# Performance work log

Hardware: AMD Instinct MI355X
Metric: run time of the kernel (lower is better)

The kernel has to match this reference:

```python
import jax, jax.numpy as jnp
import numpy as np

B, T, S = 128, 256, 64
IN, H, K, CSL, OUT = 3, 512, 10, 60, 121


def setup_inputs() -> dict:
    key = jax.random.key(0)
    ks = jax.random.split(key, 10)
    s = lambda k, shape, sc: jax.random.normal(k, shape, jnp.float32) * sc
    return {
        "x": jax.random.normal(ks[0], (B, T, IN), jnp.float32),
        "sentences": jax.random.uniform(ks[1], (B, S, CSL), dtype=jnp.float32),
        "h1_h": jnp.zeros((B, H), jnp.float32),
        "h1_c": jnp.zeros((B, H), jnp.float32),
        "h2_h": jnp.zeros((B, H), jnp.float32),
        "h2_c": jnp.zeros((B, H), jnp.float32),
        # LSTMCell params (torch gate order i,f,g,o); b = b_ih + b_hh fused
        "W_ih_cell": s(ks[2], (4 * H, IN + CSL), 0.04),
        "W_hh_cell": s(ks[3], (4 * H, H), 0.04),
        "b_cell": jnp.zeros((4 * H,), jnp.float32),
        # second-layer nn.LSTM params
        "W_ih_l": s(ks[4], (4 * H, IN + CSL + H), 0.04),
        "W_hh_l": s(ks[5], (4 * H, H), 0.04),
        "b_l": jnp.zeros((4 * H,), jnp.float32),
        # fc1 -> window params, fc2 -> output
        "W1": s(ks[6], (3 * K, H), 0.04),
        "b1": jnp.zeros((3 * K,), jnp.float32),
        "W2": s(ks[7], (OUT, H), 0.04),
        "b2": jnp.zeros((OUT,), jnp.float32),
    }


def _lstm_step(h, c, xt, W_ih, W_hh, b):
    g = xt @ W_ih.T + h @ W_hh.T + b
    i, f, gg, o = jnp.split(g, 4, axis=-1)
    c2 = jax.nn.sigmoid(f) * c + jax.nn.sigmoid(i) * jnp.tanh(gg)
    h2 = jax.nn.sigmoid(o) * jnp.tanh(c2)
    return h2, c2


def reference(x, sentences, h1_h, h1_c, h2_h, h2_c,
              W_ih_cell, W_hh_cell, b_cell,
              W_ih_l, W_hh_l, b_l, W1, b1, W2, b2):
    u = jnp.arange(1, S + 1, dtype=x.dtype)[:, None]  # [S,1] char positions

    def step1(carry, xt):
        h, c, p = carry
        ip = jnp.exp(h @ W1.T + b1)                                     # [B,3K]
        # kappa part subtracts the previous step's kappa (quirk of the source)
        p_new = jnp.concatenate([ip[:, :2 * K], ip[:, 2 * K:] - p[:, 2 * K:]], axis=-1)
        a, be, ka = jnp.split(p_new[:, None, :], 3, axis=-1)            # each [B,1,K]
        phi = (a * jnp.exp(-be * (ka - u) ** 2)).sum(-1)                # [B,S]
        win = jnp.einsum('bs,bsc->bc', phi, sentences)                  # [B,CSL]
        h2, c2 = _lstm_step(h, c, jnp.concatenate([xt, win], axis=-1),
                            W_ih_cell, W_hh_cell, b_cell)
        return (h2, c2, p_new), (h2, win)

    xs = jnp.swapaxes(x, 0, 1)                                          # [T,B,IN]
    p0 = jnp.zeros((x.shape[0], 3 * K), x.dtype)
    (h1f, c1f, _), (hx, wins) = jax.lax.scan(step1, (h1_h, h1_c, p0), xs)

    feat = jnp.concatenate([xs, wins, hx], axis=-1)                     # [T,B,IN+CSL+H]

    def step2(carry, xt):
        h, c = carry
        h2, c2 = _lstm_step(h, c, xt, W_ih_l, W_hh_l, b_l)
        return (h2, c2), h2

    (h2f, c2f), ys = jax.lax.scan(step2, (h2_h, h2_c), feat)
    y = jnp.swapaxes(ys, 0, 1).reshape(-1, H)                           # [B*T,H]
    out = y @ W2.T + b2                                                 # [B*T,OUT]
    return out, h1f, c1f, h2f, c2f
```

## Files before the change

### kernel.cpp

```cpp
#include <hip/hip_runtime.h>
#include <hip/hip_bf16.h>
#include <math.h>

typedef __attribute__((ext_vector_type(8))) short short8;
typedef __attribute__((ext_vector_type(4))) float floatx4;

#define DEVFN static __device__ __forceinline__

constexpr int B = 128, T = 256, H = 512;
constexpr int OUTW = 121;
constexpr int SLOTW = 1664;
constexpr int LOOF  = 1088;
constexpr int SLOTE = B * SLOTW;
constexpr int NSLOT = T + 2;
constexpr int NG  = 2048;
constexpr int K1  = 576,  K1C = 18;
constexpr int K2  = 1088, K2C = 34;
constexpr int KW1P = 584, KW2P = 1096;

constexpr int O_WH1 = 0;
constexpr int O_WL1 = 37376;
constexpr int O_W1S = 74752;
constexpr int O_GSM = 137152;
constexpr int O_HS  = 137152;
constexpr int O_PP  = 139264;
constexpr int O_IPL = 145472;
constexpr int O_KL  = 145592;
constexpr int O_PHL = 145632;
constexpr int O_WAC = 145888;
constexpr int O_KPR = 146848;
constexpr int O_B1S = 146888;
constexpr int O_BIA = 147008;
constexpr int O_SENT = 147136;
constexpr int O_WH2 = 0;
constexpr int O_WL2 = 70144;
constexpr int O_GS2 = 140288;
constexpr int O_BI2 = 148608;
constexpr int LDS_SZ = 162496;

DEVFN __hip_bfloat16 bhi(float v) { return __float2bfloat16(v); }
DEVFN __hip_bfloat16 blo(float v, __hip_bfloat16 h) { return __float2bfloat16(v - __bfloat162float(h)); }
DEVFN float bf2f(__hip_bfloat16 h) { return __bfloat162float(h); }
DEVFN unsigned short bbits(__hip_bfloat16 h) { union { __hip_bfloat16 h; unsigned short u; } c; c.h = h; return c.u; }
DEVFN unsigned int pack2(float a, float b) {
  return (unsigned int)bbits(bhi(a)) | ((unsigned int)bbits(bhi(b)) << 16);
}
DEVFN void ast(unsigned int* p, unsigned int v) {
  __hip_atomic_store(p, v, __ATOMIC_RELAXED, __HIP_MEMORY_SCOPE_AGENT);
}
DEVFN int ald(int* p) {
  return __hip_atomic_load(p, __ATOMIC_RELAXED, __HIP_MEMORY_SCOPE_AGENT);
}

DEVFN void waitflags(int* flags, int n, int target) {
  if ((int)threadIdx.x < n) {
    int g = 0;
    while (ald(&flags[threadIdx.x]) < target && g < (1 << 22)) { ++g; __builtin_amdgcn_s_sleep(1); }
  }
  asm volatile("" ::: "memory");
  __syncthreads();
}
DEVFN void dualwait(int* fa, int* fb, int target) {
  int tid = threadIdx.x;
  if (tid < 128) {
    int* f = (tid < 64) ? fa + tid : fb + (tid - 64);
    int g = 0;
    while (ald(f) < target && g < (1 << 22)) { ++g; __builtin_amdgcn_s_sleep(1); }
  }
  asm volatile("" ::: "memory");
  __syncthreads();
}
DEVFN void flag_store(int* flag, int val) {
  asm volatile("s_waitcnt vmcnt(0)" ::: "memory");
  __syncthreads();
  if (threadIdx.x == 0)
    __hip_atomic_store(flag, val, __ATOMIC_RELAXED, __HIP_MEMORY_SCOPE_AGENT);
}

__global__ __launch_bounds__(256) void k_pre(
    const float* __restrict__ x, const float* __restrict__ h1h, const float* __restrict__ h2h,
    const float* __restrict__ Wihc, const float* __restrict__ Whhc, const float* __restrict__ bc,
    const float* __restrict__ Wihl, const float* __restrict__ Whhl, const float* __restrict__ bl,
    const float* __restrict__ W2,
    __hip_bfloat16* __restrict__ fxHL,
    __hip_bfloat16* __restrict__ wc1, __hip_bfloat16* __restrict__ wc1l,
    __hip_bfloat16* __restrict__ wc2, __hip_bfloat16* __restrict__ wc2l,
    __hip_bfloat16* __restrict__ w2b, float* __restrict__ bi1, float* __restrict__ bi2,
    int* __restrict__ ctl)
{
  int idx = blockIdx.x * 256 + threadIdx.x;
  const int nwc1 = NG * K1, nwc2 = NG * K2, nw2b = 128 * 512, nbi = 2 * NG;
  const int nfh = B * H, nxj = T * B, nctl = 512;
  if (idx < nwc1) {
    int n = idx / K1, col = idx - n * K1;
    int src = (n & 3) * H + (n >> 2);
    float v = (col < 63) ? Wihc[src * 63 + col]
            : (col == 63 ? 0.f : Whhc[src * 512 + (col - 64)]);
    __hip_bfloat16 h = bhi(v);
    wc1[n * K1 + col] = h; wc1l[n * K1 + col] = blo(v, h);
    return;
  }
  idx -= nwc1;
  if (idx < nwc2) {
    int n = idx / K2, col = idx - n * K2;
    int src = (n & 3) * H + (n >> 2);
    float v;
    if (col < 63)       v = Wihl[src * 575 + col];
    else if (col == 63) v = 0.f;
    else if (col < 576) v = Wihl[src * 575 + (col - 1)];
    else                v = Whhl[src * 512 + (col - 576)];
    __hip_bfloat16 h = bhi(v);
    wc2[n * K2 + col] = h; wc2l[n * K2 + col] = blo(v, h);
    return;
  }
  idx -= nwc2;
  if (idx < nw2b) {
    int n = idx >> 9, col = idx & 511;
    w2b[idx] = bhi(n < OUTW ? W2[n * 512 + col] : 0.f);
    return;
  }
  idx -= nw2b;
  if (idx < nbi) {
    int n = idx & (NG - 1);
    int src = (n & 3) * H + (n >> 2);
    if (idx < NG) bi1[n] = bc[src]; else bi2[n] = bl[src];
    return;
  }
  idx -= nbi;
  if (idx < nfh) {
    int b = idx >> 9, j = idx & 511;
    float v = h1h[idx];
    __hip_bfloat16 h = bhi(v);
    fxHL[b * SLOTW + 64 + j] = h;
    fxHL[b * SLOTW + LOOF + 64 + j] = blo(v, h);
    return;
  }
  idx -= nfh;
  if (idx < nfh) {
    int b = idx >> 9, j = idx & 511;
    fxHL[(size_t)SLOTE + b * SLOTW + 576 + j] = bhi(h2h[idx]);
    return;
  }
  idx -= nfh;
  if (idx < nxj) {
    int t = idx >> 7, b = idx & 127;
    float x0 = x[(b * T + t) * 3 + 0], x1 = x[(b * T + t) * 3 + 1];
    unsigned int* ph = (unsigned int*)(fxHL + (size_t)(t + 1) * SLOTE + b * SLOTW);
    ph[0] = pack2(x0, x1);
    unsigned int* pl = (unsigned int*)(fxHL + (size_t)(t + 1) * SLOTE + b * SLOTW + LOOF);
    pl[0] = 0u;
    return;
  }
  idx -= nxj;
  if (idx < nctl) ctl[idx] = 0;
}

template <int KWP>
DEVFN void gemm3(int tid, const __hip_bfloat16* __restrict__ Aslot, int m0,
                 const __hip_bfloat16* __restrict__ Wh, const __hip_bfloat16* __restrict__ Wl,
                 int cbeg, int cend, floatx4& a0, floatx4& a1)
{
  const int lane = tid & 63, wv = tid >> 6;
  const int lm = lane & 15, lk = (lane >> 4) << 3;
  const __hip_bfloat16* Ar = Aslot + (size_t)(m0 + wv * 16 + lm) * SLOTW;
  const __hip_bfloat16* W0h = Wh + lm * KWP;
  const __hip_bfloat16* W1h = Wh + (16 + lm) * KWP;
  const __hip_bfloat16* W0l = Wl + lm * KWP;
  const __hip_bfloat16* W1l = Wl + (16 + lm) * KWP;
  #pragma unroll 4
  for (int c = cbeg; c < cend; ++c) {
    int col = c * 32 + lk;
    short8 va  = *(const short8*)(Ar + col);
    short8 ua  = *(const short8*)(Ar + LOOF + col);
    short8 vb0 = *(const short8*)(W0h + col);
    short8 vb1 = *(const short8*)(W1h + col);
    short8 ub0 = *(const short8*)(W0l + col);
    short8 ub1 = *(const short8*)(W1l + col);
    a0 = __builtin_amdgcn_mfma_f32_16x16x32_bf16(va, vb0, a0, 0, 0, 0);
    a1 = __builtin_amdgcn_mfma_f32_16x16x32_bf16(va, vb1, a1, 0, 0, 0);
    a0 = __builtin_amdgcn_mfma_f32_16x16x32_bf16(va, ub0, a0, 0, 0, 0);
    a1 = __builtin_amdgcn_mfma_f32_16x16x32_bf16(va, ub1, a1, 0, 0, 0);
    a0 = __builtin_amdgcn_mfma_f32_16x16x32_bf16(ua, vb0, a0, 0, 0, 0);
    a1 = __builtin_amdgcn_mfma_f32_16x16x32_bf16(ua, vb1, a1, 0, 0, 0);
  }
}

DEVFN void store_gsm(int tid, float* Gsm, floatx4 a0, floatx4 a1) {
  const int lane = tid & 63, wv = tid >> 6;
  const int lm = lane & 15, rr = (lane >> 4) << 2;
  #pragma unroll
  for (int r = 0; r < 4; ++r) {
    Gsm[lm * 65 + wv * 16 + rr + r]        = a0[r];
    Gsm[(16 + lm) * 65 + wv * 16 + rr + r] = a1[r];
  }
}

__global__ __launch_bounds__(256, 1) void k_persist(
    __hip_bfloat16* __restrict__ fxHL,
    const __hip_bfloat16* __restrict__ wc1, const __hip_bfloat16* __restrict__ wc1l,
    const __hip_bfloat16* __restrict__ wc2, const __hip_bfloat16* __restrict__ wc2l,
    const float* __restrict__ bi1, const float* __restrict__ bi2,
    const float* __restrict__ c1init, const float* __restrict__ c2init,
    const float* __restrict__ xin, const float* __restrict__ sent,
    const float* __restrict__ W1, const float* __restrict__ b1,
    int* __restrict__ ctl,
    float* __restrict__ h1f, float* __restrict__ c1f,
    float* __restrict__ h2f, float* __restrict__ c2f)
{
  extern __shared__ char sm[];
  const int gid = blockIdx.x, tid = threadIdx.x;
  const int lane = tid & 63, wv = tid >> 6;
  const int lm = lane & 15, lk = (lane >> 4) << 3;

  if (gid < 128) {
    const int nt1 = gid >> 1, mh = gid & 1;
    const int n0 = nt1 * 32, m0 = mh * 64;
    const int brow = mh * 64 + nt1;
    int* wf = ctl + mh * 64;
    int* hf = ctl + 128 + mh * 64;
    __hip_bfloat16* smWh = (__hip_bfloat16*)(sm + O_WH1);
    __hip_bfloat16* smWl = (__hip_bfloat16*)(sm + O_WL1);
    float* smW1 = (float*)(sm + O_W1S);
    float* Gsm  = (float*)(sm + O_GSM);
    float* hs   = (float*)(sm + O_HS);
    float* winv = (float*)(sm + O_HS);
    float* pp   = (float*)(sm + O_PP);
    float* ipl  = (float*)(sm + O_IPL);
    float* kl   = (float*)(sm + O_KL);
    float* phl  = (float*)(sm + O_PHL);
    float* wac  = (float*)(sm + O_WAC);
    float* kpr  = (float*)(sm + O_KPR);
    float* b1s  = (float*)(sm + O_B1S);
    float* bia  = (float*)(sm + O_BIA);
    float* ssent = (float*)(sm + O_SENT);

    for (int i = tid; i < 32 * 72; i += 256) {
      int r = i / 72, c8 = (i - r * 72) * 8;
      *(short8*)(smWh + r * KW1P + c8) = *(const short8*)(wc1  + (size_t)(n0 + r) * K1 + c8);
      *(short8*)(smWl + r * KW1P + c8) = *(const short8*)(wc1l + (size_t)(n0 + r) * K1 + c8);
    }
    for (int i = tid; i < 30 * 512; i += 256) {
      int j = i >> 9, c = i & 511;
      smW1[j * 520 + (c >> 6) * 65 + (c & 63)] = W1[i];
    }
    for (int i = tid; i < 64 * 60; i += 256)
      ssent[i] = sent[(size_t)brow * 64 * 60 + i];
    if (tid < 30) b1s[tid] = b1[tid];
    if (tid < 10) kpr[tid] = 0.f;
    if (tid < 32) bia[tid] = bi1[n0 + tid];
    __syncthreads();

    float creg[2];
    {
      int ml = tid >> 2, ppi = tid & 3;
      creg[0] = c1init[(m0 + ml) * H + nt1 * 8 + 2 * ppi + 0];
      creg[1] = c1init[(m0 + ml) * H + nt1 * 8 + 2 * ppi + 1];
    }

    const __hip_bfloat16* W0h = smWh + lm * KW1P;
    const __hip_bfloat16* W1h = smWh + (16 + lm) * KW1P;
    const __hip_bfloat16* W0l = smWl + lm * KW1P;
    const __hip_bfloat16* W1l = smWl + (16 + lm) * KW1P;

    for (int t = 0; t < T; ++t) {
      __hip_bfloat16* S1 = fxHL + (size_t)(t + 1) * SLOTE;
      __hip_bfloat16* S0 = fxHL + (size_t)t * SLOTE;

      waitflags(hf, 64, t);

      const __hip_bfloat16* wrow = S0 + (size_t)brow * SLOTW;
      __hip_bfloat16 a0h = wrow[64 + tid];
      __hip_bfloat16 a0l = wrow[LOOF + 64 + tid];
      __hip_bfloat16 a1h = wrow[64 + 256 + tid];
      __hip_bfloat16 a1l = wrow[LOOF + 64 + 256 + tid];
      float x2v = xin[(brow * T + t) * 3 + 2];
      const __hip_bfloat16* Ar = S0 + (size_t)(m0 + wv * 16 + lm) * SLOTW;
      short8 pva[16], pua[16];
      #pragma unroll
      for (int c = 0; c < 16; ++c) {
        pva[c] = *(const short8*)(Ar + (c + 2) * 32 + lk);
        pua[c] = *(const short8*)(Ar + LOOF + (c + 2) * 32 + lk);
      }
      hs[(tid >> 6) * 66 + (tid & 63)] = bf2f(a0h) + bf2f(a0l);
      hs[((tid + 256) >> 6) * 66 + (tid & 63)] = bf2f(a1h) + bf2f(a1l);
      __syncthreads();

      if (tid < 240) {
        int j = tid >> 3, p = tid & 7;
        const float* wp = smW1 + j * 520 + p * 65;
        const float* hv = hs + p * 66;
        float s = 0.f;
        #pragma unroll 8
        for (int k = 0; k < 64; ++k) s += hv[k] * wp[k];
        pp[tid] = s;
      }
      __syncthreads();
      if (tid < 30) {
        float s = b1s[tid];
        #pragma unroll
        for (int p = 0; p < 8; ++p) s += pp[tid * 8 + p];
        ipl[tid] = expf(s);
      }
      __syncthreads();
      if (tid < 10) {
        float kap = ipl[20 + tid] - kpr[tid];
        kpr[tid] = kap; kl[tid] = kap;
      }
      __syncthreads();
      if (tid < 64) {
        float u = (float)(tid + 1);
        float acc = 0.f;
        #pragma unroll
        for (int k = 0; k < 10; ++k) {
          float d = kl[k] - u;
          acc += ipl[k] * expf(-ipl[10 + k] * d * d);
        }
        phl[tid] = acc;
      }
      __syncthreads();
      if (tid < 240) {
        int c = tid >> 2, p = tid & 3;
        float acc = 0.f;
        #pragma unroll
        for (int s0 = 0; s0 < 16; ++s0)
          acc += phl[p * 16 + s0] * ssent[(p * 16 + s0) * 60 + c];
        wac[tid] = acc;
      }
      __syncthreads();
      if (tid < 60)
        winv[tid] = wac[tid * 4] + wac[tid * 4 + 1] + wac[tid * 4 + 2] + wac[tid * 4 + 3];
      __syncthreads();
      if (tid < 31) {
        int d = 1 + tid;
        int c0 = 2 * d, c1 = 2 * d + 1;
        float v0 = (c0 == 2) ? x2v : winv[c0 - 3];
        float v1 = (c1 == 63) ? 0.f : winv[c1 - 3];
        __hip_bfloat16 h0 = bhi(v0), h1v = bhi(v1);
        unsigned int* prow = (unsigned int*)(S1 + (size_t)brow * SLOTW);
        ast(prow + d, (unsigned int)bbits(h0) | ((unsigned int)bbits(h1v) << 16));
        ast(prow + (LOOF >> 1) + d,
            (unsigned int)bbits(blo(v0, h0)) | ((unsigned int)bbits(blo(v1, h1v)) << 16));
      }
      flag_store(wf + nt1, t + 1);

      floatx4 a0 = {0.f, 0.f, 0.f, 0.f}, a1 = a0;
      #pragma unroll
      for (int c = 0; c < 16; ++c) {
        int col = (c + 2) * 32 + lk;
        short8 vb0 = *(const short8*)(W0h + col);
        short8 vb1 = *(const short8*)(W1h + col);
        short8 ub0 = *(const short8*)(W0l + col);
        short8 ub1 = *(const short8*)(W1l + col);
        a0 = __builtin_amdgcn_mfma_f32_16x16x32_bf16(pva[c], vb0, a0, 0, 0, 0);
        a1 = __builtin_amdgcn_mfma_f32_16x16x32_bf16(pva[c], vb1, a1, 0, 0, 0);
        a0 = __builtin_amdgcn_mfma_f32_16x16x32_bf16(pva[c], ub0, a0, 0, 0, 0);
        a1 = __builtin_amdgcn_mfma_f32_16x16x32_bf16(pva[c], ub1, a1, 0, 0, 0);
        a0 = __builtin_amdgcn_mfma_f32_16x16x32_bf16(pua[c], vb0, a0, 0, 0, 0);
        a1 = __builtin_amdgcn_mfma_f32_16x16x32_bf16(pua[c], vb1, a1, 0, 0, 0);
      }
      waitflags(wf, 64, t + 1);
      gemm3<KW1P>(tid, S1, m0, smWh, smWl, 0, 2, a0, a1);
      store_gsm(tid, Gsm, a0, a1);
      __syncthreads();

      {
        int ml = tid >> 2, ppi = tid & 3;
        float v[2];
        #pragma unroll
        for (int j = 0; j < 2; ++j) {
          int nl = ppi * 8 + j * 4;
          float gi = Gsm[(nl + 0) * 65 + ml] + bia[nl + 0];
          float gf = Gsm[(nl + 1) * 65 + ml] + bia[nl + 1];
          float gg = Gsm[(nl + 2) * 65 + ml] + bia[nl + 2];
          float go = Gsm[(nl + 3) * 65 + ml] + bia[nl + 3];
          float ig = 1.f / (1.f + expf(-gi));
          float fg = 1.f / (1.f + expf(-gf));
          float gt = tanhf(gg);
          float og = 1.f / (1.f + expf(-go));
          float cn = fg * creg[j] + ig * gt;
          v[j] = og * tanhf(cn);
          creg[j] = cn;
        }
        __hip_bfloat16 h0 = bhi(v[0]), h1v = bhi(v[1]);
        unsigned int* prow = (unsigned int*)(S1 + (size_t)(m0 + ml) * SLOTW);
        int dw = 32 + nt1 * 4 + ppi;
        ast(prow + dw, (unsigned int)bbits(h0) | ((unsigned int)bbits(h1v) << 16));
        ast(prow + (LOOF >> 1) + dw,
            (unsigned int)bbits(blo(v[0], h0)) | ((unsigned int)bbits(blo(v[1], h1v)) << 16));
        if (t == T - 1) {
          int hg = nt1 * 8 + 2 * ppi;
          h1f[(m0 + ml) * H + hg]     = v[0];  c1f[(m0 + ml) * H + hg]     = creg[0];
          h1f[(m0 + ml) * H + hg + 1] = v[1];  c1f[(m0 + ml) * H + hg + 1] = creg[1];
        }
      }
      flag_store(hf + nt1, t + 1);
    }
  } else {
    const int g = gid - 128;
    const int nt2 = g >> 1, mh = g & 1;
    const int n0 = nt2 * 32, m0 = mh * 64;
    int* wf  = ctl + mh * 64;
    int* hf  = ctl + 128 + mh * 64;
    int* h2g = ctl + 256 + mh * 64;
    __hip_bfloat16* smWh = (__hip_bfloat16*)(sm + O_WH2);
    __hip_bfloat16* smWl = (__hip_bfloat16*)(sm + O_WL2);
    float* Gsm = (float*)(sm + O_GS2);
    float* bia = (float*)(sm + O_BI2);

    for (int i = tid; i < 32 * 136; i += 256) {
      int r = i / 136, c8 = (i - r * 136) * 8;
      *(short8*)(smWh + r * KW2P + c8) = *(const short8*)(wc2  + (size_t)(n0 + r) * K2 + c8);
      *(short8*)(smWl + r * KW2P + c8) = *(const short8*)(wc2l + (size_t)(n0 + r) * K2 + c8);
    }
    if (tid < 32) bia[tid] = bi2[n0 + tid];
    __syncthreads();

    float creg[2];
    {
      int ml = tid >> 2, ppi = tid & 3;
      creg[0] = c2init[(m0 + ml) * H + nt2 * 8 + 2 * ppi + 0];
      creg[1] = c2init[(m0 + ml) * H + nt2 * 8 + 2 * ppi + 1];
    }

    const __hip_bfloat16* W0h = smWh + lm * KW2P;
    const __hip_bfloat16* W1h = smWh + (16 + lm) * KW2P;
    const __hip_bfloat16* W0l = smWl + lm * KW2P;
    const __hip_bfloat16* W1l = smWl + (16 + lm) * KW2P;

    for (int t = 0; t < T; ++t) {
      __hip_bfloat16* S1 = fxHL + (size_t)(t + 1) * SLOTE;
      __hip_bfloat16* S2 = fxHL + (size_t)(t + 2) * SLOTE;
      const __hip_bfloat16* Ar = S1 + (size_t)(m0 + wv * 16 + lm) * SLOTW;

      waitflags(h2g, 64, t);
      short8 pv2[16];
      #pragma unroll
      for (int c = 0; c < 16; ++c)
        pv2[c] = *(const short8*)(Ar + (K1C + c) * 32 + lk);
      floatx4 a0 = {0.f, 0.f, 0.f, 0.f}, a1 = a0;
      #pragma unroll
      for (int c = 0; c < 16; ++c) {
        int col = (K1C + c) * 32 + lk;
        short8 vb0 = *(const short8*)(W0h + col);
        short8 vb1 = *(const short8*)(W1h + col);
        short8 ub0 = *(const short8*)(W0l + col);
        short8 ub1 = *(const short8*)(W1l + col);
        a0 = __builtin_amdgcn_mfma_f32_16x16x32_bf16(pv2[c], vb0, a0, 0, 0, 0);
        a1 = __builtin_amdgcn_mfma_f32_16x16x32_bf16(pv2[c], vb1, a1, 0, 0, 0);
        a0 = __builtin_amdgcn_mfma_f32_16x16x32_bf16(pv2[c], ub0, a0, 0, 0, 0);
        a1 = __builtin_amdgcn_mfma_f32_16x16x32_bf16(pv2[c], ub1, a1, 0, 0, 0);
      }
      dualwait(hf, wf, t + 1);
      short8 qv[18], qu[18];
      #pragma unroll
      for (int c = 0; c < 18; ++c) {
        qv[c] = *(const short8*)(Ar + c * 32 + lk);
        qu[c] = *(const short8*)(Ar + LOOF + c * 32 + lk);
      }
      #pragma unroll
      for (int c = 0; c < 18; ++c) {
        int col = c * 32 + lk;
        short8 vb0 = *(const short8*)(W0h + col);
        short8 vb1 = *(const short8*)(W1h + col);
        short8 ub0 = *(const short8*)(W0l + col);
        short8 ub1 = *(const short8*)(W1l + col);
        a0 = __builtin_amdgcn_mfma_f32_16x16x32_bf16(qv[c], vb0, a0, 0, 0, 0);
        a1 = __builtin_amdgcn_mfma_f32_16x16x32_bf16(qv[c], vb1, a1, 0, 0, 0);
        a0 = __builtin_amdgcn_mfma_f32_16x16x32_bf16(qv[c], ub0, a0, 0, 0, 0);
        a1 = __builtin_amdgcn_mfma_f32_16x16x32_bf16(qv[c], ub1, a1, 0, 0, 0);
        a0 = __builtin_amdgcn_mfma_f32_16x16x32_bf16(qu[c], vb0, a0, 0, 0, 0);
        a1 = __builtin_amdgcn_mfma_f32_16x16x32_bf16(qu[c], vb1, a1, 0, 0, 0);
      }
      store_gsm(tid, Gsm, a0, a1);
      __syncthreads();

      {
        int ml = tid >> 2, ppi = tid & 3;
        float v[2];
        #pragma unroll
        for (int j = 0; j < 2; ++j) {
          int nl = ppi * 8 + j * 4;
          float gi = Gsm[(nl + 0) * 65 + ml] + bia[nl + 0];
          float gf = Gsm[(nl + 1) * 65 + ml] + bia[nl + 1];
          float gg = Gsm[(nl + 2) * 65 + ml] + bia[nl + 2];
          float go = Gsm[(nl + 3) * 65 + ml] + bia[nl + 3];
          float ig = 1.f / (1.f + expf(-gi));
          float fg = 1.f / (1.f + expf(-gf));
          float gt = tanhf(gg);
          float og = 1.f / (1.f + expf(-go));
          float cn = fg * creg[j] + ig * gt;
          v[j] = og * tanhf(cn);
          creg[j] = cn;
        }
        __hip_bfloat16 h0 = bhi(v[0]), h1v = bhi(v[1]);
        unsigned int* prow = (unsigned int*)(S2 + (size_t)(m0 + ml) * SLOTW);
        int dw = 288 + nt2 * 4 + ppi;
        ast(prow + dw, (unsigned int)bbits(h0) | ((unsigned int)bbits(h1v) << 16));
        if (t == T - 1) {
          int hg = nt2 * 8 + 2 * ppi;
          h2f[(m0 + ml) * H + hg]     = v[0];  c2f[(m0 + ml) * H + hg]     = creg[0];
          h2f[(m0 + ml) * H + hg + 1] = v[1];  c2f[(m0 + ml) * H + hg + 1] = creg[1];
        }
      }
      flag_store(h2g + nt2, t + 1);
    }
  }
}

__global__ __launch_bounds__(256) void k_out(
    const __hip_bfloat16* __restrict__ fxHL, const __hip_bfloat16* __restrict__ w2b,
    const float* __restrict__ b2, float* __restrict__ dout)
{
  int bid = blockIdx.x, tid = threadIdx.x;
  int mblk = bid >> 1, nblk = bid & 1;
  int wv = tid >> 6, lane = tid & 63;
  int lm = lane & 15, lk = (lane >> 4) << 3;
  int m0 = mblk * 128 + wv * 32;
  int n0 = nblk * 64;
  int r0 = m0 + lm, r1 = m0 + 16 + lm;
  const __hip_bfloat16* a0p = fxHL + (size_t)((r0 & 255) + 2) * SLOTE + (r0 >> 8) * SLOTW + 576;
  const __hip_bfloat16* a1p = fxHL + (size_t)((r1 & 255) + 2) * SLOTE + (r1 >> 8) * SLOTW + 576;
  floatx4 zz = {0.f, 0.f, 0.f, 0.f};
  floatx4 acc[2][4];
  #pragma unroll
  for (int mt = 0; mt < 2; ++mt)
    #pragma unroll
    for (int nt = 0; nt < 4; ++nt) acc[mt][nt] = zz;
  #pragma unroll
  for (int c = 0; c < 16; ++c) {
    int col = c * 32 + lk;
    short8 va0 = *(const short8*)(a0p + col);
    short8 va1 = *(const short8*)(a1p + col);
    short8 vb[4];
    #pragma unroll
    for (int nt = 0; nt < 4; ++nt)
      vb[nt] = *(const short8*)(w2b + (size_t)(n0 + nt * 16 + lm) * 512 + col);
    #pragma unroll
    for (int nt = 0; nt < 4; ++nt) {
      acc[0][nt] = __builtin_amdgcn_mfma_f32_16x16x32_bf16(va0, vb[nt], acc[0][nt], 0, 0, 0);
      acc[1][nt] = __builtin_amdgcn_mfma_f32_16x16x32_bf16(va1, vb[nt], acc[1][nt], 0, 0, 0);
    }
  }
  int rr = (lane >> 4) << 2;
  #pragma unroll
  for (int mt = 0; mt < 2; ++mt)
    #pragma unroll
    for (int nt = 0; nt < 4; ++nt)
      #pragma unroll
      for (int r = 0; r < 4; ++r) {
        int m = m0 + mt * 16 + rr + r;
        int n = n0 + nt * 16 + lm;
        if (n < OUTW) dout[(size_t)m * OUTW + n] = acc[mt][nt][r] + b2[n];
      }
}

extern "C" void kernel_launch(void* const* d_in, const int* in_sizes, int n_in,
                              void* d_out, int out_size, void* d_ws, size_t ws_size,
                              hipStream_t stream)
{
  (void)in_sizes; (void)n_in; (void)out_size; (void)ws_size;
  const float* x    = (const float*)d_in[0];
  const float* sent = (const float*)d_in[1];
  const float* h1h  = (const float*)d_in[2];
  const float* h1c  = (const float*)d_in[3];
  const float* h2h  = (const float*)d_in[4];
  const float* h2c  = (const float*)d_in[5];
  const float* Wihc = (const float*)d_in[6];
  const float* Whhc = (const float*)d_in[7];
  const float* bc   = (const float*)d_in[8];
  const float* Wihl = (const float*)d_in[9];
  const float* Whhl = (const float*)d_in[10];
  const float* bl   = (const float*)d_in[11];
  const float* W1   = (const float*)d_in[12];
  const float* b1   = (const float*)d_in[13];
  const float* W2   = (const float*)d_in[14];
  const float* b2   = (const float*)d_in[15];

  float* out = (float*)d_out;
  float* h1f = out + (size_t)B * T * OUTW;
  float* c1f = h1f + (size_t)B * H;
  float* h2f = c1f + (size_t)B * H;
  float* c2f = h2f + (size_t)B * H;

  char* p = (char*)d_ws;
  auto carve = [&](size_t bytes) { char* r = p; p += (bytes + 255) & ~(size_t)255; return r; };
  __hip_bfloat16* fxHL = (__hip_bfloat16*)carve((size_t)NSLOT * SLOTE * 2);
  __hip_bfloat16* wc1  = (__hip_bfloat16*)carve((size_t)NG * K1 * 2);
  __hip_bfloat16* wc1l = (__hip_bfloat16*)carve((size_t)NG * K1 * 2);
  __hip_bfloat16* wc2  = (__hip_bfloat16*)carve((size_t)NG * K2 * 2);
  __hip_bfloat16* wc2l = (__hip_bfloat16*)carve((size_t)NG * K2 * 2);
  __hip_bfloat16* w2b  = (__hip_bfloat16*)carve((size_t)128 * 512 * 2);
  float* bi1 = (float*)carve((size_t)NG * 4);
  float* bi2 = (float*)carve((size_t)NG * 4);
  int*   ctl = (int*)carve((size_t)512 * 4);

  static bool attr_set = false;
  if (!attr_set) {
    (void)hipFuncSetAttribute((const void*)k_persist,
                              hipFuncAttributeMaxDynamicSharedMemorySize, LDS_SZ);
    attr_set = true;
  }

  k_pre<<<14226, 256, 0, stream>>>(x, h1h, h2h, Wihc, Whhc, bc, Wihl, Whhl, bl, W2,
                                   fxHL, wc1, wc1l, wc2, wc2l, w2b, bi1, bi2, ctl);
  k_persist<<<256, 256, LDS_SZ, stream>>>(fxHL, wc1, wc1l, wc2, wc2l, bi1, bi2,
                                          h1c, h2c, x, sent, W1, b1, ctl,
                                          h1f, c1f, h2f, c2f);
  k_out<<<512, 256, 0, stream>>>(fxHL, w2b, b2, out);
}
```

Measured before the change: 2.966 ms.

## Replace window-ready flag barriers with per-word sentinel polling on data

Removes the separate window-ready flag and its grid-wide wait. Consumers instead poll the window data words themselves until a sentinel value (0x7FFF7FFF, pre-filled by a new k_sent kernel) is overwritten. The remaining hidden-state flags are padded to a stride of 4 ints to cut false sharing. This drops one cross-block barrier per timestep on the serial recurrence path. In exchange it adds a full sentinel-fill kernel over the workspace, relies on the sentinel never matching a real bf16 pair, and uses per-word relaxed atomic loads whose visibility ordering is fragile.

```diff
diff --git a/kernel.cpp b/kernel.cpp
--- a/kernel.cpp
+++ b/kernel.cpp
@@ -17,6 +17,8 @@
 constexpr int K1  = 576,  K1C = 18;
 constexpr int K2  = 1088, K2C = 34;
 constexpr int KW1P = 584, KW2P = 1096;
+constexpr int FSTR = 4;
+constexpr unsigned int SENT = 0x7FFF7FFFu;
 
 constexpr int O_WH1 = 0;
 constexpr int O_WL1 = 37376;
@@ -41,6 +43,9 @@
 DEVFN __hip_bfloat16 bhi(float v) { return __float2bfloat16(v); }
 DEVFN __hip_bfloat16 blo(float v, __hip_bfloat16 h) { return __float2bfloat16(v - __bfloat162float(h)); }
 DEVFN float bf2f(__hip_bfloat16 h) { return __bfloat162float(h); }
+DEVFN float bfu(unsigned short u) {
+  union { unsigned short u; __hip_bfloat16 h; } c; c.u = u; return __bfloat162float(c.h);
+}
 DEVFN unsigned short bbits(__hip_bfloat16 h) { union { __hip_bfloat16 h; unsigned short u; } c; c.h = h; return c.u; }
 DEVFN unsigned int pack2(float a, float b) {
   return (unsigned int)bbits(bhi(a)) | ((unsigned int)bbits(bhi(b)) << 16);
@@ -51,21 +56,14 @@
 DEVFN int ald(int* p) {
   return __hip_atomic_load(p, __ATOMIC_RELAXED, __HIP_MEMORY_SCOPE_AGENT);
 }
+DEVFN unsigned int uald(const unsigned int* p) {
+  return __hip_atomic_load((unsigned int*)p, __ATOMIC_RELAXED, __HIP_MEMORY_SCOPE_AGENT);
+}
 
 DEVFN void waitflags(int* flags, int n, int target) {
   if ((int)threadIdx.x < n) {
     int g = 0;
-    while (ald(&flags[threadIdx.x]) < target && g < (1 << 22)) { ++g; __builtin_amdgcn_s_sleep(1); }
-  }
-  asm volatile("" ::: "memory");
-  __syncthreads();
-}
-DEVFN void dualwait(int* fa, int* fb, int target) {
-  int tid = threadIdx.x;
-  if (tid < 128) {
-    int* f = (tid < 64) ? fa + tid : fb + (tid - 64);
-    int g = 0;
-    while (ald(f) < target && g < (1 << 22)) { ++g; __builtin_amdgcn_s_sleep(1); }
+    while (ald(&flags[threadIdx.x * FSTR]) < target && g < (1 << 22)) { ++g; __builtin_amdgcn_s_sleep(1); }
   }
   asm volatile("" ::: "memory");
   __syncthreads();
@@ -75,6 +73,18 @@
   __syncthreads();
   if (threadIdx.x == 0)
     __hip_atomic_store(flag, val, __ATOMIC_RELAXED, __HIP_MEMORY_SCOPE_AGENT);
+}
+
+__global__ __launch_bounds__(256) void k_sent(__hip_bfloat16* __restrict__ fxHL)
+{
+  int blk = blockIdx.x;
+  int slot = (blk >> 7) + 1;
+  int row  = blk & 127;
+  unsigned int* rb = (unsigned int*)(fxHL + (size_t)slot * SLOTE + (size_t)row * SLOTW);
+  for (int i = threadIdx.x; i < 287; i += 256) {
+    rb[1 + i] = SENT;
+    rb[(LOOF >> 1) + 1 + i] = SENT;
+  }
 }
 
 __global__ __launch_bounds__(256) void k_pre(
@@ -90,7 +100,7 @@
 {
   int idx = blockIdx.x * 256 + threadIdx.x;
   const int nwc1 = NG * K1, nwc2 = NG * K2, nw2b = 128 * 512, nbi = 2 * NG;
-  const int nfh = B * H, nxj = T * B, nctl = 512;
+  const int nfh = B * H, nxj = T * B, nctl = 1024;
   if (idx < nwc1) {
     int n = idx / K1, col = idx - n * K1;
     int src = (n & 3) * H + (n >> 2);
@@ -153,36 +163,6 @@
   }
   idx -= nxj;
   if (idx < nctl) ctl[idx] = 0;
-}
-
-template <int KWP>
-DEVFN void gemm3(int tid, const __hip_bfloat16* __restrict__ Aslot, int m0,
-                 const __hip_bfloat16* __restrict__ Wh, const __hip_bfloat16* __restrict__ Wl,
-                 int cbeg, int cend, floatx4& a0, floatx4& a1)
-{
-  const int lane = tid & 63, wv = tid >> 6;
-  const int lm = lane & 15, lk = (lane >> 4) << 3;
-  const __hip_bfloat16* Ar = Aslot + (size_t)(m0 + wv * 16 + lm) * SLOTW;
-  const __hip_bfloat16* W0h = Wh + lm * KWP;
-  const __hip_bfloat16* W1h = Wh + (16 + lm) * KWP;
-  const __hip_bfloat16* W0l = Wl + lm * KWP;
-  const __hip_bfloat16* W1l = Wl + (16 + lm) * KWP;
-  #pragma unroll 4
-  for (int c = cbeg; c < cend; ++c) {
-    int col = c * 32 + lk;
-    short8 va  = *(const short8*)(Ar + col);
-    short8 ua  = *(const short8*)(Ar + LOOF + col);
-    short8 vb0 = *(const short8*)(W0h + col);
-    short8 vb1 = *(const short8*)(W1h + col);
-    short8 ub0 = *(const short8*)(W0l + col);
-    short8 ub1 = *(const short8*)(W1l + col);
-    a0 = __builtin_amdgcn_mfma_f32_16x16x32_bf16(va, vb0, a0, 0, 0, 0);
-    a1 = __builtin_amdgcn_mfma_f32_16x16x32_bf16(va, vb1, a1, 0, 0, 0);
-    a0 = __builtin_amdgcn_mfma_f32_16x16x32_bf16(va, ub0, a0, 0, 0, 0);
-    a1 = __builtin_amdgcn_mfma_f32_16x16x32_bf16(va, ub1, a1, 0, 0, 0);
-    a0 = __builtin_amdgcn_mfma_f32_16x16x32_bf16(ua, vb0, a0, 0, 0, 0);
-    a1 = __builtin_amdgcn_mfma_f32_16x16x32_bf16(ua, vb1, a1, 0, 0, 0);
-  }
 }
 
 DEVFN void store_gsm(int tid, float* Gsm, floatx4 a0, floatx4 a1) {
@@ -216,8 +196,7 @@
     const int nt1 = gid >> 1, mh = gid & 1;
     const int n0 = nt1 * 32, m0 = mh * 64;
     const int brow = mh * 64 + nt1;
-    int* wf = ctl + mh * 64;
-    int* hf = ctl + 128 + mh * 64;
+    int* hf = ctl + mh * 256;
     __hip_bfloat16* smWh = (__hip_bfloat16*)(sm + O_WH1);
     __hip_bfloat16* smWl = (__hip_bfloat16*)(sm + O_WL1);
     float* smW1 = (float*)(sm + O_W1S);
@@ -266,14 +245,28 @@
       __hip_bfloat16* S1 = fxHL + (size_t)(t + 1) * SLOTE;
       __hip_bfloat16* S0 = fxHL + (size_t)t * SLOTE;
 
+      float x2v = xin[(brow * T + t) * 3 + 2];
+
+      {
+        const unsigned int* rb = (const unsigned int*)(S0 + (size_t)brow * SLOTW);
+        const unsigned int* hp = rb + 32 + tid;
+        const unsigned int* lp = rb + (LOOF >> 1) + 32 + tid;
+        unsigned int hw = uald(hp), lw = uald(lp);
+        int g = 0;
+        while ((hw == SENT || lw == SENT) && g < (1 << 22)) {
+          __builtin_amdgcn_s_sleep(1);
+          if (hw == SENT) hw = uald(hp);
+          if (lw == SENT) lw = uald(lp);
+          ++g;
+        }
+        int c0 = 2 * tid;
+        float v0 = bfu((unsigned short)(hw & 0xFFFFu)) + bfu((unsigned short)(lw & 0xFFFFu));
+        float v1 = bfu((unsigned short)(hw >> 16)) + bfu((unsigned short)(lw >> 16));
+        hs[(c0 >> 6) * 66 + (c0 & 63)] = v0;
+        hs[((c0 + 1) >> 6) * 66 + ((c0 + 1) & 63)] = v1;
+      }
+
       waitflags(hf, 64, t);
-
-      const __hip_bfloat16* wrow = S0 + (size_t)brow * SLOTW;
-      __hip_bfloat16 a0h = wrow[64 + tid];
-      __hip_bfloat16 a0l = wrow[LOOF + 64 + tid];
-      __hip_bfloat16 a1h = wrow[64 + 256 + tid];
-      __hip_bfloat16 a1l = wrow[LOOF + 64 + 256 + tid];
-      float x2v = xin[(brow * T + t) * 3 + 2];
       const __hip_bfloat16* Ar = S0 + (size_t)(m0 + wv * 16 + lm) * SLOTW;
       short8 pva[16], pua[16];
       #pragma unroll
@@ -281,9 +274,6 @@
         pva[c] = *(const short8*)(Ar + (c + 2) * 32 + lk);
         pua[c] = *(const short8*)(Ar + LOOF + (c + 2) * 32 + lk);
       }
-      hs[(tid >> 6) * 66 + (tid & 63)] = bf2f(a0h) + bf2f(a0l);
-      hs[((tid + 256) >> 6) * 66 + (tid & 63)] = bf2f(a1h) + bf2f(a1l);
-      __syncthreads();
 
       if (tid < 240) {
         int j = tid >> 3, p = tid & 7;
@@ -341,7 +331,6 @@
         ast(prow + (LOOF >> 1) + d,
             (unsigned int)bbits(blo(v0, h0)) | ((unsigned int)bbits(blo(v1, h1v)) << 16));
       }
-      flag_store(wf + nt1, t + 1);
 
       floatx4 a0 = {0.f, 0.f, 0.f, 0.f}, a1 = a0;
       #pragma unroll
@@ -358,8 +347,53 @@
         a0 = __builtin_amdgcn_mfma_f32_16x16x32_bf16(pua[c], vb0, a0, 0, 0, 0);
         a1 = __builtin_amdgcn_mfma_f32_16x16x32_bf16(pua[c], vb1, a1, 0, 0, 0);
       }
-      waitflags(wf, 64, t + 1);
-      gemm3<KW1P>(tid, S1, m0, smWh, smWl, 0, 2, a0, a1);
+
+      {
+        const unsigned int* wb = (const unsigned int*)(S1 + (size_t)(m0 + wv * 16 + lm) * SLOTW);
+        const int dq = lk >> 1;
+        unsigned int d[16];
+        #pragma unroll
+        for (int c = 0; c < 2; ++c)
+          #pragma unroll
+          for (int q = 0; q < 4; ++q) {
+            d[c * 4 + q]     = uald(wb + c * 16 + dq + q);
+            d[8 + c * 4 + q] = uald(wb + (LOOF >> 1) + c * 16 + dq + q);
+          }
+        int g = 0;
+        for (;;) {
+          bool any = false;
+          #pragma unroll
+          for (int j = 0; j < 16; ++j) if (d[j] == SENT) any = true;
+          if (!any || g >= (1 << 22)) break;
+          __builtin_amdgcn_s_sleep(1);
+          #pragma unroll
+          for (int c = 0; c < 2; ++c)
+            #pragma unroll
+            for (int q = 0; q < 4; ++q) {
+              if (d[c * 4 + q] == SENT)     d[c * 4 + q]     = uald(wb + c * 16 + dq + q);
+              if (d[8 + c * 4 + q] == SENT) d[8 + c * 4 + q] = uald(wb + (LOOF >> 1) + c * 16 + dq + q);
+            }
+          ++g;
+        }
+        union U4 { unsigned int u[4]; short8 s; };
+        #pragma unroll
+        for (int c = 0; c < 2; ++c) {
+          U4 va, ua;
+          #pragma unroll
+          for (int q = 0; q < 4; ++q) { va.u[q] = d[c * 4 + q]; ua.u[q] = d[8 + c * 4 + q]; }
+          int col = c * 32 + lk;
+          short8 vb0 = *(const short8*)(W0h + col);
+          short8 vb1 = *(const short8*)(W1h + col);
+          short8 ub0 = *(const short8*)(W0l + col);
+          short8 ub1 = *(const short8*)(W1l + col);
+          a0 = __builtin_amdgcn_mfma_f32_16x16x32_bf16(va.s, vb0, a0, 0, 0, 0);
+          a1 = __builtin_amdgcn_mfma_f32_16x16x32_bf16(va.s, vb1, a1, 0, 0, 0);
+          a0 = __builtin_amdgcn_mfma_f32_16x16x32_bf16(va.s, ub0, a0, 0, 0, 0);
+          a1 = __builtin_amdgcn_mfma_f32_16x16x32_bf16(va.s, ub1, a1, 0, 0, 0);
+          a0 = __builtin_amdgcn_mfma_f32_16x16x32_bf16(ua.s, vb0, a0, 0, 0, 0);
+          a1 = __builtin_amdgcn_mfma_f32_16x16x32_bf16(ua.s, vb1, a1, 0, 0, 0);
+        }
+      }
       store_gsm(tid, Gsm, a0, a1);
       __syncthreads();
 
@@ -393,15 +427,14 @@
           h1f[(m0 + ml) * H + hg + 1] = v[1];  c1f[(m0 + ml) * H + hg + 1] = creg[1];
         }
       }
-      flag_store(hf + nt1, t + 1);
+      flag_store(hf + nt1 * FSTR, t + 1);
     }
   } else {
-    const int g = gid - 128;
-    const int nt2 = g >> 1, mh = g & 1;
+    const int g2 = gid - 128;
+    const int nt2 = g2 >> 1, mh = g2 & 1;
     const int n0 = nt2 * 32, m0 = mh * 64;
-    int* wf  = ctl + mh * 64;
-    int* hf  = ctl + 128 + mh * 64;
-    int* h2g = ctl + 256 + mh * 64;
+    int* hf  = ctl + mh * 256;
+    int* h2g = ctl + 512 + mh * 256;
     __hip_bfloat16* smWh = (__hip_bfloat16*)(sm + O_WH2);
     __hip_bfloat16* smWl = (__hip_bfloat16*)(sm + O_WL2);
     float* Gsm = (float*)(sm + O_GS2);
@@ -450,7 +483,7 @@
         a0 = __builtin_amdgcn_mfma_f32_16x16x32_bf16(pv2[c], ub0, a0, 0, 0, 0);
         a1 = __builtin_amdgcn_mfma_f32_16x16x32_bf16(pv2[c], ub1, a1, 0, 0, 0);
       }
-      dualwait(hf, wf, t + 1);
+      waitflags(hf, 64, t + 1);
       short8 qv[18], qu[18];
       #pragma unroll
       for (int c = 0; c < 18; ++c) {
@@ -502,7 +535,7 @@
           h2f[(m0 + ml) * H + hg + 1] = v[1];  c2f[(m0 + ml) * H + hg + 1] = creg[1];
         }
       }
-      flag_store(h2g + nt2, t + 1);
+      flag_store(h2g + nt2 * FSTR, t + 1);
     }
   }
 }
@@ -592,7 +625,7 @@
   __hip_bfloat16* w2b  = (__hip_bfloat16*)carve((size_t)128 * 512 * 2);
   float* bi1 = (float*)carve((size_t)NG * 4);
   float* bi2 = (float*)carve((size_t)NG * 4);
-  int*   ctl = (int*)carve((size_t)512 * 4);
+  int*   ctl = (int*)carve((size_t)1024 * 4);
 
   static bool attr_set = false;
   if (!attr_set) {
@@ -601,7 +634,8 @@
     attr_set = true;
   }
 
-  k_pre<<<14226, 256, 0, stream>>>(x, h1h, h2h, Wihc, Whhc, bc, Wihl, Whhl, bl, W2,
+  k_sent<<<32768, 256, 0, stream>>>(fxHL);
+  k_pre<<<14228, 256, 0, stream>>>(x, h1h, h2h, Wihc, Whhc, bc, Wihl, Whhl, bl, W2,
                                    fxHL, wc1, wc1l, wc2, wc2l, w2b, bi1, bi2, ctl);
   k_persist<<<256, 256, LDS_SZ, stream>>>(fxHL, wc1, wc1l, wc2, wc2l, bi1, bi2,
                                           h1c, h2c, x, sent, W1, b1, ctl,
```

Result: faster. 2.894 ms (-2.4%).
